# Performance work log

Hardware: AMD Instinct MI355X
Metric: run time of the kernel (lower is better)

## Reference

```python
import jax, jax.numpy as jnp
import numpy as np

EPS = 1e-5
N_HEADS = 8

def layer_norm(x, g, b):
    mu = x.mean(-1, keepdims=True)
    var = ((x - mu) ** 2).mean(-1, keepdims=True)
    return (x - mu) * jax.lax.rsqrt(var + EPS) * g + b

def rotate_half(x):
    d = x.shape[-1] // 2
    return jnp.concatenate([-x[..., d:], x[..., :d]], axis=-1)

def setup_inputs() -> dict:
    key = jax.random.key(0)
    ks = jax.random.split(key, 6)
    b, n, m, h, dh = 4, 512, 8192, N_HEADS, 16
    dim = h * dh
    s = dim ** -0.5
    return {
        "x": jax.random.normal(ks[0], (b, n, dim), jnp.float32),
        "mem_kv": jax.random.normal(ks[1], (b, h, m, 2 * dh), jnp.float32),
        "w_q": jax.random.normal(ks[2], (dim, dim), jnp.float32) * s,
        "w_kv": jax.random.normal(ks[3], (2 * dim, dim), jnp.float32) * s,
        "w_out": jax.random.normal(ks[4], (dim, dim), jnp.float32) * s,
        "b_out": jnp.zeros((dim,), jnp.float32),
        "g1": jnp.ones((dim,), jnp.float32),
        "b1": jnp.zeros((dim,), jnp.float32),
        "g2": jnp.ones((dim,), jnp.float32),
        "b2": jnp.zeros((dim,), jnp.float32),
    }

def reference(x, mem_kv, w_q, w_kv, w_out, b_out, g1, b1, g2, b2):
    b, n, dim = x.shape
    h = N_HEADS
    dh = dim // h
    # pre-norm + projections
    x_ = layer_norm(x, g1, b1)
    q = (x_ @ w_q.T).reshape(b, n, h, dh).transpose(0, 2, 1, 3)          # [b,h,n,dh]
    kv = (x_ @ w_kv.T).reshape(b, n, h, 2 * dh).transpose(0, 2, 1, 3)    # [b,h,n,2dh]
    mem_kv = jnp.concatenate([mem_kv, kv], axis=2)                        # growing cache
    k, v = jnp.split(mem_kv, 2, axis=-1)                                  # [b,h,j,dh] each
    q = q * dh ** -0.5
    # rotary embeddings (SinusoidalEmbeddings over k length, q uses trailing n positions)
    j = k.shape[2]
    inv_freq = 1.0 / (10000.0 ** (jnp.arange(0, dh, 2, dtype=jnp.float32) / dh))
    fr = jnp.arange(j, dtype=jnp.float32)[:, None] * inv_freq[None, :]
    freqs = jnp.concatenate([fr, fr], axis=-1)                            # [j, dh]
    cos, sin = jnp.cos(freqs), jnp.sin(freqs)
    q = q * cos[-n:] + rotate_half(q) * sin[-n:]
    k = k * cos + rotate_half(k) * sin
    # full attention of new chunk over cache (forward_simple, inference)
    sim = jnp.einsum('bhie,bhje->bhij', q, k)
    attn = jax.nn.softmax(sim, axis=-1)
    hv = jnp.einsum('bhij,bhje->bhie', attn, v)
    hv = hv.transpose(0, 2, 1, 3).reshape(b, n, dim) + x                  # residual
    out = layer_norm(hv, g2, b2) @ w_out.T + b_out + hv                   # out proj + residual
    return out, mem_kv
```

## Files before the change

### kernel.cpp

```cpp
#include <hip/hip_runtime.h>

#define B 4
#define N 512
#define M 8192
#define H 8
#define DH 16
#define DIM 128
#define J (M + N)
#define LN10000_DIV8 1.1512925465f
#define LOG2E 1.44269504f

typedef _Float16 f16;
typedef _Float16 half4 __attribute__((ext_vector_type(4)));
typedef _Float16 half8 __attribute__((ext_vector_type(8)));
typedef __fp16 fp16x2 __attribute__((ext_vector_type(2)));
typedef float f32x4 __attribute__((ext_vector_type(4)));

#if __has_builtin(__builtin_amdgcn_exp2f)
#define EXP2(x) __builtin_amdgcn_exp2f(x)
#else
#define EXP2(x) exp2f(x)
#endif

union PK { fp16x2 v; unsigned int u; };

__device__ __forceinline__ half8 pack8(float a, float b, float c, float d,
                                       float e, float f, float g, float h) {
#if __has_builtin(__builtin_amdgcn_cvt_pkrtz)
    union { unsigned int u[4]; half8 h8; } r;
    PK p0, p1, p2, p3;
    p0.v = __builtin_amdgcn_cvt_pkrtz(a, b);
    p1.v = __builtin_amdgcn_cvt_pkrtz(c, d);
    p2.v = __builtin_amdgcn_cvt_pkrtz(e, f);
    p3.v = __builtin_amdgcn_cvt_pkrtz(g, h);
    r.u[0] = p0.u; r.u[1] = p1.u; r.u[2] = p2.u; r.u[3] = p3.u;
    return r.h8;
#else
    half8 r = { (f16)a, (f16)b, (f16)c, (f16)d, (f16)e, (f16)f, (f16)g, (f16)h };
    return r;
#endif
}

#define WS_KROT 0ull
#define WS_VT   8912896ull
#define WS_QROT 17825792ull
#define WS_HV   18350080ull
#define WS_XN   18874368ull

union V4  { f16 h[4];  uint2 u; };

__device__ __forceinline__ half8 cvt8(const float* p) {
    float4 a = *(const float4*)p, b = *(const float4*)(p + 4);
    half8 h = { (f16)a.x, (f16)a.y, (f16)a.z, (f16)a.w,
                (f16)b.x, (f16)b.y, (f16)b.z, (f16)b.w };
    return h;
}

__global__ void prep_kernel(const float4* __restrict__ src, float4* __restrict__ dst,
                            f16* __restrict__ krot, f16* __restrict__ vt,
                            const float* __restrict__ x, const float* __restrict__ g1,
                            const float* __restrict__ b1, f16* __restrict__ xn16)
{
    if (blockIdx.x < 4096) {
        __shared__ float tile[64][33];
        int bh = blockIdx.x >> 7;
        int j0 = (blockIdx.x & 127) * 64;
        int t = threadIdx.x;

        #pragma unroll
        for (int rep = 0; rep < 2; rep++) {
            int idx = t + rep * 256;
            int row = idx >> 3, c4 = idx & 7;
            float4 v = src[((size_t)bh * M + j0 + row) * 8 + c4];
            dst[((size_t)bh * J + j0 + row) * 8 + c4] = v;
            tile[row][c4 * 4 + 0] = v.x; tile[row][c4 * 4 + 1] = v.y;
            tile[row][c4 * 4 + 2] = v.z; tile[row][c4 * 4 + 3] = v.w;
        }
        __syncthreads();

        if (t < 128) {
            int row = t >> 1, rh = t & 1;
            int j = j0 + row;
            float lo4[4], hi4[4];
            #pragma unroll
            for (int i = 0; i < 4; i++) {
                int r = rh * 4 + i;
                float ang = (float)j * __expf(-(float)r * LN10000_DIV8);
                float sn, cs; __sincosf(ang, &sn, &cs);
                float lo = tile[row][r], hi = tile[row][r + 8];
                lo4[i] = lo * cs - hi * sn;
                hi4[i] = hi * cs + lo * sn;
            }
            int tilei = j >> 5, jj = j & 31;
            int col4 = (jj >> 3) * 4 + (jj & 3), frag = (jj >> 2) & 1;
            f16* base = krot + (size_t)bh * J * 16 + (size_t)tilei * 512 + col4 * 8 + frag * 4;
            V4 wl, wh;
            #pragma unroll
            for (int i = 0; i < 4; i++) { wl.h[i] = (f16)lo4[i]; wh.h[i] = (f16)hi4[i]; }
            *(uint2*)(base + rh * 128)       = wl.u;
            *(uint2*)(base + (2 + rh) * 128) = wh.u;
        }
        {
            int dh = t >> 4, c0 = (t & 15) * 4;
            V4 vv;
            #pragma unroll
            for (int i = 0; i < 4; i++) vv.h[i] = (f16)tile[c0 + i][16 + dh];
            *(uint2*)(vt + (size_t)bh * 16 * J + (size_t)dh * J + j0 + c0) = vv.u;
        }
    } else {
        int wave = threadIdx.x >> 6, lane = threadIdx.x & 63;
        int token = (blockIdx.x - 4096) * 4 + wave;
        float v0 = x[(size_t)token * DIM + lane];
        float v1 = x[(size_t)token * DIM + lane + 64];
        float s = v0 + v1;
        for (int off = 32; off; off >>= 1) s += __shfl_xor(s, off, 64);
        float mu = s * (1.0f / DIM);
        float d0 = v0 - mu, d1 = v1 - mu;
        float vs = d0 * d0 + d1 * d1;
        for (int off = 32; off; off >>= 1) vs += __shfl_xor(vs, off, 64);
        float rs = rsqrtf(vs * (1.0f / DIM) + 1e-5f);
        xn16[(size_t)token * DIM + lane]      = (f16)(d0 * rs * g1[lane]      + b1[lane]);
        xn16[(size_t)token * DIM + lane + 64] = (f16)(d1 * rs * g1[lane + 64] + b1[lane + 64]);
    }
}

__global__ void __launch_bounds__(256) proj_kernel(
    const f16* __restrict__ xn16, const float* __restrict__ wq,
    const float* __restrict__ wkv, float* __restrict__ out_mem,
    f16* __restrict__ krot, f16* __restrict__ vt, f16* __restrict__ qrot)
{
    int id = blockIdx.x * 4 + (threadIdx.x >> 6);
    int lane = threadIdx.x & 63;
    int ttile = id & 127, ctile = id >> 7;
    int token0 = ttile * 16;
    int col = lane & 15, quad = lane >> 4;

    const float* wbase = (ctile < 8) ? (wq + (size_t)(ctile * 16 + col) * DIM)
                                     : (wkv + (size_t)((ctile - 8) * 16 + col) * DIM);
    const f16* abase = xn16 + (size_t)(token0 + col) * DIM + quad * 8;

    f32x4 acc = {0.f, 0.f, 0.f, 0.f};
    #pragma unroll
    for (int kb = 0; kb < 4; kb++) {
        half8 a = *(const half8*)(abase + kb * 32);
        half8 w = cvt8(wbase + kb * 32 + quad * 8);
        acc = __builtin_amdgcn_mfma_f32_16x16x32_f16(a, w, acc, 0, 0, 0);
    }

    int e = col, r8 = e & 7;
    float f = __expf(-(float)r8 * LN10000_DIV8);
    int kt = ctile - 8;
    int head = (ctile < 8) ? ctile : (kt >> 1);
    int isV  = (ctile >= 8) ? (kt & 1) : 0;

    #pragma unroll
    for (int r = 0; r < 4; r++) {
        int tok = token0 + quad * 4 + r;
        int b = tok >> 9, i = tok & (N - 1);
        int bhh = b * H + head;
        float self = acc[r];
        float prt = __shfl_xor(self, 8, 64);

        if (ctile < 8) {
            float ang = (float)(M + i) * f;
            float sn, cs; __sincosf(ang, &sn, &cs);
            float rv = (self * cs + ((e < 8) ? -prt : prt) * sn) * (0.25f * LOG2E);
            qrot[((size_t)bhh * N + i) * 16 + e] = (f16)rv;
        } else if (!isV) {
            out_mem[((size_t)bhh * J + M + i) * 32 + e] = self;
            float ang = (float)(M + i) * f;
            float sn, cs; __sincosf(ang, &sn, &cs);
            float rv = self * cs + ((e < 8) ? -prt : prt) * sn;
            int jpos = M + i;
            int tilei = jpos >> 5, jj = jpos & 31;
            int col4 = (jj >> 3) * 4 + (jj & 3), frag = (jj >> 2) & 1;
            krot[(size_t)bhh * J * 16 + (size_t)tilei * 512 +
                 (e >> 2) * 128 + col4 * 8 + frag * 4 + (e & 3)] = (f16)rv;
        } else {
            out_mem[((size_t)bhh * J + M + i) * 32 + 16 + e] = self;
            vt[(size_t)bhh * 16 * J + (size_t)e * J + M + i] = (f16)self;
        }
    }
}

__global__ void __launch_bounds__(1024) attn_kernel(
    const f16* __restrict__ krot, const f16* __restrict__ vt,
    const f16* __restrict__ qrot, f16* __restrict__ hvw)
{
    __shared__ float sacc[16][2][256];
    __shared__ float sl[16][2][16];
    int bh = blockIdx.x & 31;
    int q0 = (blockIdx.x >> 5) * 32;
    int wave = threadIdx.x >> 6, lane = threadIdx.x & 63;
    int col = lane & 15, quad = lane >> 4;

    const f16* vb = vt + (size_t)bh * 16 * J + (size_t)col * J;
    half4 qfa = *(const half4*)(qrot + ((size_t)bh * N + q0 + col) * 16 + quad * 4);
    half4 qfb = *(const half4*)(qrot + ((size_t)bh * N + q0 + 16 + col) * 16 + quad * 4);

    int jstart = wave * (J / 16);
    const f16* kptr = krot + (size_t)bh * J * 16 + (size_t)jstart * 16 + lane * 8;
    const f16* vptr = vb + jstart + quad * 8;

    f32x4 acca = {0.f, 0.f, 0.f, 0.f};
    f32x4 accb = {0.f, 0.f, 0.f, 0.f};
    f32x4 accla = {0.f, 0.f, 0.f, 0.f};
    f32x4 acclb = {0.f, 0.f, 0.f, 0.f};
    const f32x4 zero = {0.f, 0.f, 0.f, 0.f};
    const half8 ones = { (f16)1.f, (f16)1.f, (f16)1.f, (f16)1.f,
                         (f16)1.f, (f16)1.f, (f16)1.f, (f16)1.f };

    #pragma unroll 2
    for (int it = 0; it < 17; ++it) {
        half8 kf8 = *(const half8*)kptr;
        half8 vf  = *(const half8*)vptr;
        kptr += 512; vptr += 32;
        half4 kf0 = __builtin_shufflevector(kf8, kf8, 0, 1, 2, 3);
        half4 kf1 = __builtin_shufflevector(kf8, kf8, 4, 5, 6, 7);
        f32x4 s0a = __builtin_amdgcn_mfma_f32_16x16x16f16(kf0, qfa, zero, 0, 0, 0);
        f32x4 s1a = __builtin_amdgcn_mfma_f32_16x16x16f16(kf1, qfa, zero, 0, 0, 0);
        f32x4 s0b = __builtin_amdgcn_mfma_f32_16x16x16f16(kf0, qfb, zero, 0, 0, 0);
        f32x4 s1b = __builtin_amdgcn_mfma_f32_16x16x16f16(kf1, qfb, zero, 0, 0, 0);

        float a0 = EXP2(s0a[0]), a1 = EXP2(s0a[1]), a2 = EXP2(s0a[2]), a3 = EXP2(s0a[3]);
        float a4 = EXP2(s1a[0]), a5 = EXP2(s1a[1]), a6 = EXP2(s1a[2]), a7 = EXP2(s1a[3]);
        float b0 = EXP2(s0b[0]), b1 = EXP2(s0b[1]), b2 = EXP2(s0b[2]), b3 = EXP2(s0b[3]);
        float b4 = EXP2(s1b[0]), b5 = EXP2(s1b[1]), b6 = EXP2(s1b[2]), b7 = EXP2(s1b[3]);
        half8 pfa = pack8(a0, a1, a2, a3, a4, a5, a6, a7);
        half8 pfb = pack8(b0, b1, b2, b3, b4, b5, b6, b7);
        acca  = __builtin_amdgcn_mfma_f32_16x16x32_f16(pfa, vf,   acca,  0, 0, 0);
        accla = __builtin_amdgcn_mfma_f32_16x16x32_f16(pfa, ones, accla, 0, 0, 0);
        accb  = __builtin_amdgcn_mfma_f32_16x16x32_f16(pfb, vf,   accb,  0, 0, 0);
        acclb = __builtin_amdgcn_mfma_f32_16x16x32_f16(pfb, ones, acclb, 0, 0, 0);
    }

    if (col == 0) {
        #pragma unroll
        for (int r = 0; r < 4; r++) {
            sl[wave][0][quad * 4 + r] = accla[r];
            sl[wave][1][quad * 4 + r] = acclb[r];
        }
    }
    #pragma unroll
    for (int r = 0; r < 4; r++) {
        sacc[wave][0][(quad * 4 + r) * 16 + col] = acca[r];
        sacc[wave][1][(quad * 4 + r) * 16 + col] = accb[r];
    }
    __syncthreads();

    if (wave < 2) {
        int qt = wave;
        int b = bh >> 3, h = bh & 7;
        #pragma unroll
        for (int r = 0; r < 4; r++) {
            int ql = quad * 4 + r;
            float o = 0.f, lt = 0.f;
            #pragma unroll
            for (int w = 0; w < 16; w++) {
                o  += sacc[w][qt][ql * 16 + col];
                lt += sl[w][qt][ql];
            }
            hvw[((size_t)(b * N) + q0 + qt * 16 + ql) * DIM + h * DH + col] = (f16)(o / lt);
        }
    }
}

__global__ void __launch_bounds__(256) final_kernel(
    const f16* __restrict__ hvw, const float* __restrict__ x,
    const float* __restrict__ wout, const float* __restrict__ bout,
    const float* __restrict__ g2, const float* __restrict__ b2v,
    float* __restrict__ out)
{
    __shared__ f16 xn2[16][136];
    __shared__ float hres[16][132];
    int token0 = (blockIdx.x >> 1) * 16;
    int half = blockIdx.x & 1;
    int wave = threadIdx.x >> 6, lane = threadIdx.x & 63;

    #pragma unroll
    for (int tt = 0; tt < 4; tt++) {
        int tl = wave * 4 + tt;
        int token = token0 + tl;
        float h0 = (float)hvw[(size_t)token * DIM + lane]      + x[(size_t)token * DIM + lane];
        float h1 = (float)hvw[(size_t)token * DIM + lane + 64] + x[(size_t)token * DIM + lane + 64];
        float s = h0 + h1;
        for (int off = 32; off; off >>= 1) s += __shfl_xor(s, off, 64);
        float mu = s * (1.0f / DIM);
        float d0 = h0 - mu, d1 = h1 - mu;
        float vs = d0 * d0 + d1 * d1;
        for (int off = 32; off; off >>= 1) vs += __shfl_xor(vs, off, 64);
        float rs = rsqrtf(vs * (1.0f / DIM) + 1e-5f);
        xn2[tl][lane]      = (f16)(d0 * rs * g2[lane]      + b2v[lane]);
        xn2[tl][lane + 64] = (f16)(d1 * rs * g2[lane + 64] + b2v[lane + 64]);
        hres[tl][lane] = h0; hres[tl][lane + 64] = h1;
    }
    __syncthreads();

    int col = lane & 15, quad = lane >> 4;
    int ct = half * 4 + wave;
    int cg = ct * 16 + col;
    const float* wrow = wout + (size_t)cg * DIM;
    f32x4 acc = {0.f, 0.f, 0.f, 0.f};
    #pragma unroll
    for (int kb = 0; kb < 4; kb++) {
        half8 a = *(const half8*)(&xn2[col][kb * 32 + quad * 8]);
        half8 w = cvt8(wrow + kb * 32 + quad * 8);
        acc = __builtin_amdgcn_mfma_f32_16x16x32_f16(a, w, acc, 0, 0, 0);
    }
    float bo = bout[cg];
    #pragma unroll
    for (int r = 0; r < 4; r++) {
        int tl = quad * 4 + r;
        out[(size_t)(token0 + tl) * DIM + cg] = acc[r] + bo + hres[tl][cg];
    }
}

extern "C" void kernel_launch(void* const* d_in, const int* in_sizes, int n_in,
                              void* d_out, int out_size, void* d_ws, size_t ws_size,
                              hipStream_t stream)
{
    const float* x      = (const float*)d_in[0];
    const float* mem_kv = (const float*)d_in[1];
    const float* wq     = (const float*)d_in[2];
    const float* wkv    = (const float*)d_in[3];
    const float* wout   = (const float*)d_in[4];
    const float* bout   = (const float*)d_in[5];
    const float* g1     = (const float*)d_in[6];
    const float* b1     = (const float*)d_in[7];
    const float* g2     = (const float*)d_in[8];
    const float* b2     = (const float*)d_in[9];

    float* out = (float*)d_out;
    float* out_mem = out + (size_t)B * N * DIM;

    f16* krot = (f16*)((char*)d_ws + WS_KROT);
    f16* vt   = (f16*)((char*)d_ws + WS_VT);
    f16* qrot = (f16*)((char*)d_ws + WS_QROT);
    f16* hvw  = (f16*)((char*)d_ws + WS_HV);
    f16* xn16 = (f16*)((char*)d_ws + WS_XN);

    hipLaunchKernelGGL(prep_kernel, dim3(4608), dim3(256), 0, stream,
                       (const float4*)mem_kv, (float4*)out_mem, krot, vt,
                       x, g1, b1, xn16);
    hipLaunchKernelGGL(proj_kernel, dim3(768), dim3(256), 0, stream,
                       xn16, wq, wkv, out_mem, krot, vt, qrot);
    hipLaunchKernelGGL(attn_kernel, dim3(512), dim3(1024), 0, stream,
                       krot, vt, qrot, hvw);
    hipLaunchKernelGGL(final_kernel, dim3(256), dim3(256), 0, stream,
                       hvw, x, wout, bout, g2, b2, out);
}
```

Before: 141.6 us.

## Split layernorm out, fuse projection with cache copy, nontemporal stores, parallel reduce

Layer norm now runs in its own small kernel, and the projection is merged into the large cache-copy/rotary kernel. The projection blocks come first in the grid so they can overlap with the memory-bound copy. The copy of mem_kv into the output uses nontemporal stores to avoid polluting cache. The attention epilogue spreads the cross-wave reduction over 512 threads instead of 2 waves, shortening the serial tail per block. The kernel count stays at four.

```diff
diff --git a/kernel.cpp b/kernel.cpp
--- a/kernel.cpp
+++ b/kernel.cpp
@@ -56,15 +56,90 @@
     return h;
 }
 
-__global__ void prep_kernel(const float4* __restrict__ src, float4* __restrict__ dst,
-                            f16* __restrict__ krot, f16* __restrict__ vt,
-                            const float* __restrict__ x, const float* __restrict__ g1,
-                            const float* __restrict__ b1, f16* __restrict__ xn16)
-{
-    if (blockIdx.x < 4096) {
+__global__ void __launch_bounds__(256) ln_kernel(
+    const float* __restrict__ x, const float* __restrict__ g1,
+    const float* __restrict__ b1, f16* __restrict__ xn16)
+{
+    int wave = threadIdx.x >> 6, lane = threadIdx.x & 63;
+    int token = blockIdx.x * 4 + wave;
+    float v0 = x[(size_t)token * DIM + lane];
+    float v1 = x[(size_t)token * DIM + lane + 64];
+    float s = v0 + v1;
+    for (int off = 32; off; off >>= 1) s += __shfl_xor(s, off, 64);
+    float mu = s * (1.0f / DIM);
+    float d0 = v0 - mu, d1 = v1 - mu;
+    float vs = d0 * d0 + d1 * d1;
+    for (int off = 32; off; off >>= 1) vs += __shfl_xor(vs, off, 64);
+    float rs = rsqrtf(vs * (1.0f / DIM) + 1e-5f);
+    xn16[(size_t)token * DIM + lane]      = (f16)(d0 * rs * g1[lane]      + b1[lane]);
+    xn16[(size_t)token * DIM + lane + 64] = (f16)(d1 * rs * g1[lane + 64] + b1[lane + 64]);
+}
+
+__global__ void __launch_bounds__(256) prep_proj_kernel(
+    const float4* __restrict__ src, float4* __restrict__ dstv,
+    f16* __restrict__ krot, f16* __restrict__ vt,
+    const f16* __restrict__ xn16, const float* __restrict__ wq,
+    const float* __restrict__ wkv, f16* __restrict__ qrot)
+{
+    if (blockIdx.x < 768) {
+        float* out_mem = (float*)dstv;
+        int id = blockIdx.x * 4 + (threadIdx.x >> 6);
+        int lane = threadIdx.x & 63;
+        int ttile = id & 127, ctile = id >> 7;
+        int token0 = ttile * 16;
+        int col = lane & 15, quad = lane >> 4;
+
+        const float* wbase = (ctile < 8) ? (wq + (size_t)(ctile * 16 + col) * DIM)
+                                         : (wkv + (size_t)((ctile - 8) * 16 + col) * DIM);
+        const f16* abase = xn16 + (size_t)(token0 + col) * DIM + quad * 8;
+
+        f32x4 acc = {0.f, 0.f, 0.f, 0.f};
+        #pragma unroll
+        for (int kb = 0; kb < 4; kb++) {
+            half8 a = *(const half8*)(abase + kb * 32);
+            half8 w = cvt8(wbase + kb * 32 + quad * 8);
+            acc = __builtin_amdgcn_mfma_f32_16x16x32_f16(a, w, acc, 0, 0, 0);
+        }
+
+        int e = col, r8 = e & 7;
+        float f = __expf(-(float)r8 * LN10000_DIV8);
+        int kt = ctile - 8;
+        int head = (ctile < 8) ? ctile : (kt >> 1);
+        int isV  = (ctile >= 8) ? (kt & 1) : 0;
+
+        #pragma unroll
+        for (int r = 0; r < 4; r++) {
+            int tok = token0 + quad * 4 + r;
+            int b = tok >> 9, i = tok & (N - 1);
+            int bhh = b * H + head;
+            float self = acc[r];
+            float prt = __shfl_xor(self, 8, 64);
+
+            if (ctile < 8) {
+                float ang = (float)(M + i) * f;
+                float sn, cs; __sincosf(ang, &sn, &cs);
+                float rv = (self * cs + ((e < 8) ? -prt : prt) * sn) * (0.25f * LOG2E);
+                qrot[((size_t)bhh * N + i) * 16 + e] = (f16)rv;
+            } else if (!isV) {
+                out_mem[((size_t)bhh * J + M + i) * 32 + e] = self;
+                float ang = (float)(M + i) * f;
+                float sn, cs; __sincosf(ang, &sn, &cs);
+                float rv = self * cs + ((e < 8) ? -prt : prt) * sn;
+                int jpos = M + i;
+                int tilei = jpos >> 5, jj = jpos & 31;
+                int col4 = (jj >> 3) * 4 + (jj & 3), frag = (jj >> 2) & 1;
+                krot[(size_t)bhh * J * 16 + (size_t)tilei * 512 +
+                     (e >> 2) * 128 + col4 * 8 + frag * 4 + (e & 3)] = (f16)rv;
+            } else {
+                out_mem[((size_t)bhh * J + M + i) * 32 + 16 + e] = self;
+                vt[(size_t)bhh * 16 * J + (size_t)e * J + M + i] = (f16)self;
+            }
+        }
+    } else {
         __shared__ float tile[64][33];
-        int bh = blockIdx.x >> 7;
-        int j0 = (blockIdx.x & 127) * 64;
+        int bid = blockIdx.x - 768;
+        int bh = bid >> 7;
+        int j0 = (bid & 127) * 64;
         int t = threadIdx.x;
 
         #pragma unroll
@@ -72,7 +147,9 @@
             int idx = t + rep * 256;
             int row = idx >> 3, c4 = idx & 7;
             float4 v = src[((size_t)bh * M + j0 + row) * 8 + c4];
-            dst[((size_t)bh * J + j0 + row) * 8 + c4] = v;
+            f32x4 vv = { v.x, v.y, v.z, v.w };
+            __builtin_nontemporal_store(vv,
+                (f32x4*)dstv + ((size_t)bh * J + j0 + row) * 8 + c4);
             tile[row][c4 * 4 + 0] = v.x; tile[row][c4 * 4 + 1] = v.y;
             tile[row][c4 * 4 + 2] = v.z; tile[row][c4 * 4 + 3] = v.w;
         }
@@ -107,79 +184,6 @@
             for (int i = 0; i < 4; i++) vv.h[i] = (f16)tile[c0 + i][16 + dh];
             *(uint2*)(vt + (size_t)bh * 16 * J + (size_t)dh * J + j0 + c0) = vv.u;
         }
-    } else {
-        int wave = threadIdx.x >> 6, lane = threadIdx.x & 63;
-        int token = (blockIdx.x - 4096) * 4 + wave;
-        float v0 = x[(size_t)token * DIM + lane];
-        float v1 = x[(size_t)token * DIM + lane + 64];
-        float s = v0 + v1;
-        for (int off = 32; off; off >>= 1) s += __shfl_xor(s, off, 64);
-        float mu = s * (1.0f / DIM);
-        float d0 = v0 - mu, d1 = v1 - mu;
-        float vs = d0 * d0 + d1 * d1;
-        for (int off = 32; off; off >>= 1) vs += __shfl_xor(vs, off, 64);
-        float rs = rsqrtf(vs * (1.0f / DIM) + 1e-5f);
-        xn16[(size_t)token * DIM + lane]      = (f16)(d0 * rs * g1[lane]      + b1[lane]);
-        xn16[(size_t)token * DIM + lane + 64] = (f16)(d1 * rs * g1[lane + 64] + b1[lane + 64]);
-    }
-}
-
-__global__ void __launch_bounds__(256) proj_kernel(
-    const f16* __restrict__ xn16, const float* __restrict__ wq,
-    const float* __restrict__ wkv, float* __restrict__ out_mem,
-    f16* __restrict__ krot, f16* __restrict__ vt, f16* __restrict__ qrot)
-{
-    int id = blockIdx.x * 4 + (threadIdx.x >> 6);
-    int lane = threadIdx.x & 63;
-    int ttile = id & 127, ctile = id >> 7;
-    int token0 = ttile * 16;
-    int col = lane & 15, quad = lane >> 4;
-
-    const float* wbase = (ctile < 8) ? (wq + (size_t)(ctile * 16 + col) * DIM)
-                                     : (wkv + (size_t)((ctile - 8) * 16 + col) * DIM);
-    const f16* abase = xn16 + (size_t)(token0 + col) * DIM + quad * 8;
-
-    f32x4 acc = {0.f, 0.f, 0.f, 0.f};
-    #pragma unroll
-    for (int kb = 0; kb < 4; kb++) {
-        half8 a = *(const half8*)(abase + kb * 32);
-        half8 w = cvt8(wbase + kb * 32 + quad * 8);
-        acc = __builtin_amdgcn_mfma_f32_16x16x32_f16(a, w, acc, 0, 0, 0);
-    }
-
-    int e = col, r8 = e & 7;
-    float f = __expf(-(float)r8 * LN10000_DIV8);
-    int kt = ctile - 8;
-    int head = (ctile < 8) ? ctile : (kt >> 1);
-    int isV  = (ctile >= 8) ? (kt & 1) : 0;
-
-    #pragma unroll
-    for (int r = 0; r < 4; r++) {
-        int tok = token0 + quad * 4 + r;
-        int b = tok >> 9, i = tok & (N - 1);
-        int bhh = b * H + head;
-        float self = acc[r];
-        float prt = __shfl_xor(self, 8, 64);
-
-        if (ctile < 8) {
-            float ang = (float)(M + i) * f;
-            float sn, cs; __sincosf(ang, &sn, &cs);
-            float rv = (self * cs + ((e < 8) ? -prt : prt) * sn) * (0.25f * LOG2E);
-            qrot[((size_t)bhh * N + i) * 16 + e] = (f16)rv;
-        } else if (!isV) {
-            out_mem[((size_t)bhh * J + M + i) * 32 + e] = self;
-            float ang = (float)(M + i) * f;
-            float sn, cs; __sincosf(ang, &sn, &cs);
-            float rv = self * cs + ((e < 8) ? -prt : prt) * sn;
-            int jpos = M + i;
-            int tilei = jpos >> 5, jj = jpos & 31;
-            int col4 = (jj >> 3) * 4 + (jj & 3), frag = (jj >> 2) & 1;
-            krot[(size_t)bhh * J * 16 + (size_t)tilei * 512 +
-                 (e >> 2) * 128 + col4 * 8 + frag * 4 + (e & 3)] = (f16)rv;
-        } else {
-            out_mem[((size_t)bhh * J + M + i) * 32 + 16 + e] = self;
-            vt[(size_t)bhh * 16 * J + (size_t)e * J + M + i] = (f16)self;
-        }
     }
 }
 
@@ -248,20 +252,17 @@
     }
     __syncthreads();
 
-    if (wave < 2) {
-        int qt = wave;
+    if (threadIdx.x < 512) {
+        int t = threadIdx.x;
+        int qt = t >> 8, ql = (t >> 4) & 15, c = t & 15;
+        float o = 0.f, lt = 0.f;
+        #pragma unroll
+        for (int w = 0; w < 16; w++) {
+            o  += sacc[w][qt][ql * 16 + c];
+            lt += sl[w][qt][ql];
+        }
         int b = bh >> 3, h = bh & 7;
-        #pragma unroll
-        for (int r = 0; r < 4; r++) {
-            int ql = quad * 4 + r;
-            float o = 0.f, lt = 0.f;
-            #pragma unroll
-            for (int w = 0; w < 16; w++) {
-                o  += sacc[w][qt][ql * 16 + col];
-                lt += sl[w][qt][ql];
-            }
-            hvw[((size_t)(b * N) + q0 + qt * 16 + ql) * DIM + h * DH + col] = (f16)(o / lt);
-        }
+        hvw[((size_t)(b * N) + q0 + qt * 16 + ql) * DIM + h * DH + c] = (f16)(o / lt);
     }
 }
 
@@ -339,11 +340,11 @@
     f16* hvw  = (f16*)((char*)d_ws + WS_HV);
     f16* xn16 = (f16*)((char*)d_ws + WS_XN);
 
-    hipLaunchKernelGGL(prep_kernel, dim3(4608), dim3(256), 0, stream,
+    hipLaunchKernelGGL(ln_kernel, dim3(512), dim3(256), 0, stream,
+                       x, g1, b1, xn16);
+    hipLaunchKernelGGL(prep_proj_kernel, dim3(4864), dim3(256), 0, stream,
                        (const float4*)mem_kv, (float4*)out_mem, krot, vt,
-                       x, g1, b1, xn16);
-    hipLaunchKernelGGL(proj_kernel, dim3(768), dim3(256), 0, stream,
-                       xn16, wq, wkv, out_mem, krot, vt, qrot);
+                       xn16, wq, wkv, qrot);
     hipLaunchKernelGGL(attn_kernel, dim3(512), dim3(1024), 0, stream,
                        krot, vt, qrot, hvw);
     hipLaunchKernelGGL(final_kernel, dim3(256), dim3(256), 0, stream,
```

After: 138.2 us. 2.4% less time.
